# Kernel optimization log

Hardware: AMD Instinct MI355X
Metric: run time of the kernel (lower is better)

Reference implementation:

```python
import jax, jax.numpy as jnp
import numpy as np

N_STATE = 1024
N_HEAD = 16
HEAD_DIM = N_STATE // N_HEAD
SEQLENS = [1024, 896, 768, 640, 512, 384, 896, 1024]  # sum = 6144
TOTAL = sum(SEQLENS)


def setup_inputs() -> dict:
    key = jax.random.key(0)
    ks = jax.random.split(key, 8)
    s = 0.02
    cu = jnp.asarray(np.concatenate([[0], np.cumsum(SEQLENS)]), dtype=jnp.int32)
    return {
        "x": jax.random.normal(ks[0], (TOTAL, N_STATE), jnp.float32),
        "cu_seqlens": cu,
        "Wq": jax.random.normal(ks[1], (N_STATE, N_STATE), jnp.float32) * s,
        "bq": jax.random.normal(ks[2], (N_STATE,), jnp.float32) * s,
        "Wk": jax.random.normal(ks[3], (N_STATE, N_STATE), jnp.float32) * s,
        "Wv": jax.random.normal(ks[4], (N_STATE, N_STATE), jnp.float32) * s,
        "bv": jax.random.normal(ks[5], (N_STATE,), jnp.float32) * s,
        "Wo": jax.random.normal(ks[6], (N_STATE, N_STATE), jnp.float32) * s,
        "bo": jax.random.normal(ks[7], (N_STATE,), jnp.float32) * s,
    }


def reference(x, cu_seqlens, Wq, bq, Wk, Wv, bv, Wo, bo):
    # cu_seqlens is a static (host) quantity in the original (used via .tolist())
    cu = np.asarray(jax.device_get(cu_seqlens))
    seqlens = cu[1:] - cu[:-1]
    B = len(seqlens)
    Lmax = int(seqlens.max())

    q = x @ Wq.T + bq              # [T, n_state]
    k = x @ Wk.T                   # key has no bias
    v = x @ Wv.T + bv

    # static pad/unpad index maps (honoring the ragged structure)
    ar = np.arange(Lmax)
    valid = ar[None, :] < seqlens[:, None]             # [B, Lmax]
    idx = np.where(valid, cu[:-1, None] + ar[None, :], 0)
    unpad_idx = np.nonzero(valid.reshape(-1))[0]       # flat positions of real tokens
    valid_j = jnp.asarray(valid)

    def pad(t):  # [T, n_state] -> [B, Lmax, H, D], zeros in padding
        p = jnp.where(valid_j[:, :, None], t[idx], 0.0)
        return p.reshape(B, Lmax, N_HEAD, HEAD_DIM)

    qp, kp, vp = pad(q), pad(k), pad(v)
    scale = HEAD_DIM ** -0.5
    # torch adds the bool mask (True->1.0) after masked_fill(mask==0, -max):
    # valid keys get +1.0 (softmax-invariant shift), invalid keys get -finfo.max
    big_neg = jnp.finfo(x.dtype).max
    add_mask = jnp.where(valid_j, 1.0, -big_neg)[:, None, None, :]  # [B,1,1,Lmax]

    scores = jnp.einsum("bqhd,bkhd->bhqk", qp, kp) * scale + add_mask
    weights = jax.nn.softmax(scores, axis=-1)
    ctx = jnp.einsum("bhqk,bkhd->bqhd", weights, vp)   # [B, Lmax, H, D]
    ctx_flat = ctx.reshape(B * Lmax, N_STATE)[unpad_idx]  # [T, n_state]
    return ctx_flat @ Wo.T + bo
```

## Files before the change

kernel.cpp:

```cpp
#include <hip/hip_runtime.h>

typedef unsigned short u16;
typedef unsigned int u32;
typedef __attribute__((ext_vector_type(8))) short bf16x8;
typedef __attribute__((ext_vector_type(4))) float f32x4;

#define MFMA_BF16(a, b, c) __builtin_amdgcn_mfma_f32_16x16x32_bf16((a), (b), (c), 0, 0, 0)

#define QSCALE 0.18033688011112042f

__device__ __forceinline__ u16 f2bf(float f) {
    union { float f; unsigned u; } v; v.f = f;
    return (u16)((v.u + 0x7FFFu + ((v.u >> 16) & 1u)) >> 16);
}

__device__ __forceinline__ u32 cvtpk(float a, float b) {
    u32 r;
    asm("v_cvt_pk_bf16_f32 %0, %1, %2" : "=v"(r) : "v"(a), "v"(b));
    return r;
}

__device__ __forceinline__ void async16(const void* g, void* l) {
    __builtin_amdgcn_global_load_lds(
        (const __attribute__((address_space(1))) void*)g,
        (__attribute__((address_space(3))) void*)l, 16, 0, 0);
}

__global__ __launch_bounds__(256) void cvt_all(
    const float* __restrict__ x, const float* __restrict__ Wq, const float* __restrict__ Wk,
    const float* __restrict__ Wv, const float* __restrict__ Wo,
    u16* __restrict__ xb, u16* __restrict__ Wqb, u16* __restrict__ Wkb,
    u16* __restrict__ Wvb, u16* __restrict__ Wob) {
    int b = blockIdx.x;
    const float* src; u16* dst; int base;
    if (b < 6144)      { src = x;  dst = xb;  base = b; }
    else if (b < 7168) { src = Wq; dst = Wqb; base = b - 6144; }
    else if (b < 8192) { src = Wk; dst = Wkb; base = b - 7168; }
    else if (b < 9216) { src = Wv; dst = Wvb; base = b - 8192; }
    else               { src = Wo; dst = Wob; base = b - 9216; }
    int i = base * 256 + threadIdx.x;
    float4 v = ((const float4*)src)[i];
    unsigned long long pk = (unsigned long long)f2bf(v.x)
                          | ((unsigned long long)f2bf(v.y) << 16)
                          | ((unsigned long long)f2bf(v.z) << 32)
                          | ((unsigned long long)f2bf(v.w) << 48);
    *(unsigned long long*)(dst + (size_t)i * 4) = pk;
}

__global__ __launch_bounds__(512) void gemm_qkv(
    const u16* __restrict__ xb,
    const u16* __restrict__ Wqb, const u16* __restrict__ Wkb, const u16* __restrict__ Wvb,
    const float* __restrict__ bq, const float* __restrict__ bv,
    u16* __restrict__ qb, u16* __restrict__ kb, u16* __restrict__ vbT) {
    __shared__ __align__(16) u16 As[2][128 * 64];
    __shared__ __align__(16) u16 Bs[2][128 * 64];
    const int tid = threadIdx.x;

    const int fid = blockIdx.x;
    const int xcd = fid & 7;
    const int slot = fid >> 3;
    const int mloc = slot % 6;
    const int nidx = slot / 6;
    const int m0 = (xcd * 6 + mloc) << 7;
    const int buf = nidx >> 3;
    const int n0 = (nidx & 7) << 7;
    const u16* __restrict__ W = (buf == 0) ? Wqb : (buf == 1) ? Wkb : Wvb;

    const int rr = tid >> 3;
    const int cg = tid & 7;
    const int wv = tid >> 6, lane = tid & 63, g = lane >> 4, c = lane & 15;
    const int wm = (wv & 1) << 6;
    const int wn = (wv >> 1) << 5;

    const int sw = (cg ^ (rr & 7)) << 3;
    const u16* gA[2]; const u16* gB[2];
#pragma unroll
    for (int r = 0; r < 2; ++r) {
        gA[r] = xb + (size_t)(m0 + (r << 6) + rr) * 1024 + sw;
        gB[r] = W + (size_t)(n0 + (r << 6) + rr) * 1024 + sw;
    }

    f32x4 zero = {0.f, 0.f, 0.f, 0.f};
    f32x4 acc[4][2];
#pragma unroll
    for (int i = 0; i < 4; ++i)
#pragma unroll
        for (int j = 0; j < 2; ++j) acc[i][j] = zero;

#pragma unroll
    for (int r = 0; r < 2; ++r) {
        async16(gA[r], &As[0][(r << 12) + tid * 8]);
        async16(gB[r], &Bs[0][(r << 12) + tid * 8]);
    }
#pragma unroll
    for (int r = 0; r < 2; ++r) {
        async16(gA[r] + 64, &As[1][(r << 12) + tid * 8]);
        async16(gB[r] + 64, &Bs[1][(r << 12) + tid * 8]);
    }
    asm volatile("s_waitcnt vmcnt(4)" ::: "memory");
    __builtin_amdgcn_s_barrier();
    __builtin_amdgcn_sched_barrier(0);

    for (int kt = 0; kt < 16; ++kt) {
        const int cur = kt & 1;
#pragma unroll
        for (int ks = 0; ks < 2; ++ks) {
            bf16x8 af[4], bb[2];
#pragma unroll
            for (int i = 0; i < 4; ++i) {
                int ra = wm + (i << 4) + c;
                af[i] = *(const bf16x8*)(&As[cur][ra * 64 + ((((ks << 2) + g) ^ (ra & 7)) << 3)]);
            }
#pragma unroll
            for (int j = 0; j < 2; ++j) {
                int rb = wn + (j << 4) + c;
                bb[j] = *(const bf16x8*)(&Bs[cur][rb * 64 + ((((ks << 2) + g) ^ (rb & 7)) << 3)]);
            }
#pragma unroll
            for (int i = 0; i < 4; ++i)
#pragma unroll
                for (int j = 0; j < 2; ++j) acc[i][j] = MFMA_BF16(af[i], bb[j], acc[i][j]);
        }
        if (kt == 15) break;
        __builtin_amdgcn_sched_barrier(0);
        __builtin_amdgcn_s_barrier();
        if (kt < 14) {
            const int k0 = (kt + 2) << 6;
#pragma unroll
            for (int r = 0; r < 2; ++r) {
                async16(gA[r] + k0, &As[cur][(r << 12) + tid * 8]);
                async16(gB[r] + k0, &Bs[cur][(r << 12) + tid * 8]);
            }
            asm volatile("s_waitcnt vmcnt(4)" ::: "memory");
        } else {
            asm volatile("s_waitcnt vmcnt(0)" ::: "memory");
        }
        __builtin_amdgcn_s_barrier();
        __builtin_amdgcn_sched_barrier(0);
    }

    if (buf == 0) {
#pragma unroll
        for (int j = 0; j < 2; ++j) {
            int col = n0 + wn + (j << 4) + c;
            float bias = bq[col];
#pragma unroll
            for (int i = 0; i < 4; ++i) {
                int rowb = m0 + wm + (i << 4) + (g << 2);
#pragma unroll
                for (int r = 0; r < 4; ++r)
                    qb[(size_t)(rowb + r) * 1024 + col] = f2bf((acc[i][j][r] + bias) * QSCALE);
            }
        }
    } else if (buf == 1) {
#pragma unroll
        for (int j = 0; j < 2; ++j) {
            int col = n0 + wn + (j << 4) + c;
#pragma unroll
            for (int i = 0; i < 4; ++i) {
                int rowb = m0 + wm + (i << 4) + (g << 2);
#pragma unroll
                for (int r = 0; r < 4; ++r)
                    kb[(size_t)(rowb + r) * 1024 + col] = f2bf(acc[i][j][r]);
            }
        }
    } else {
#pragma unroll
        for (int j = 0; j < 2; ++j) {
            int col = n0 + wn + (j << 4) + c;
            float bias = bv[col];
#pragma unroll
            for (int i = 0; i < 4; ++i) {
                int trow = m0 + wm + (i << 4) + (g << 2);
                unsigned long long pk =
                      (unsigned long long)f2bf(acc[i][j][0] + bias)
                    | ((unsigned long long)f2bf(acc[i][j][1] + bias) << 16)
                    | ((unsigned long long)f2bf(acc[i][j][2] + bias) << 32)
                    | ((unsigned long long)f2bf(acc[i][j][3] + bias) << 48);
                *(unsigned long long*)(vbT + (size_t)col * 6144 + trow) = pk;
            }
        }
    }
}

__global__ __launch_bounds__(512) void gemm_out(
    const u16* __restrict__ ctxb, const u16* __restrict__ Wob,
    const float* __restrict__ bo, float* __restrict__ out) {
    __shared__ __align__(16) u16 As[2][128 * 64];
    __shared__ __align__(16) u16 Bs[2][128 * 64];
    const int tid = threadIdx.x;

    const int fid = blockIdx.x;
    const int xcd = fid & 7;
    const int slot = fid >> 3;
    const int mloc = slot % 6;
    const int nidx = slot / 6;
    const int m0 = (xcd * 6 + mloc) << 7;
    const int n0 = nidx << 7;

    const int rr = tid >> 3, cg = tid & 7;
    const int wv = tid >> 6, lane = tid & 63, g = lane >> 4, c = lane & 15;
    const int wm = (wv & 1) << 6;
    const int wn = (wv >> 1) << 5;

    const int sw = (cg ^ (rr & 7)) << 3;
    const u16* gA[2]; const u16* gB[2];
#pragma unroll
    for (int r = 0; r < 2; ++r) {
        gA[r] = ctxb + (size_t)(m0 + (r << 6) + rr) * 1024 + sw;
        gB[r] = Wob + (size_t)(n0 + (r << 6) + rr) * 1024 + sw;
    }

    f32x4 zero = {0.f, 0.f, 0.f, 0.f};
    f32x4 acc[4][2];
#pragma unroll
    for (int i = 0; i < 4; ++i)
#pragma unroll
        for (int j = 0; j < 2; ++j) acc[i][j] = zero;

#pragma unroll
    for (int r = 0; r < 2; ++r) {
        async16(gA[r], &As[0][(r << 12) + tid * 8]);
        async16(gB[r], &Bs[0][(r << 12) + tid * 8]);
    }
#pragma unroll
    for (int r = 0; r < 2; ++r) {
        async16(gA[r] + 64, &As[1][(r << 12) + tid * 8]);
        async16(gB[r] + 64, &Bs[1][(r << 12) + tid * 8]);
    }
    asm volatile("s_waitcnt vmcnt(4)" ::: "memory");
    __builtin_amdgcn_s_barrier();
    __builtin_amdgcn_sched_barrier(0);

    for (int kt = 0; kt < 16; ++kt) {
        const int cur = kt & 1;
#pragma unroll
        for (int ks = 0; ks < 2; ++ks) {
            bf16x8 af[4], bb[2];
#pragma unroll
            for (int i = 0; i < 4; ++i) {
                int ra = wm + (i << 4) + c;
                af[i] = *(const bf16x8*)(&As[cur][ra * 64 + ((((ks << 2) + g) ^ (ra & 7)) << 3)]);
            }
#pragma unroll
            for (int j = 0; j < 2; ++j) {
                int rb = wn + (j << 4) + c;
                bb[j] = *(const bf16x8*)(&Bs[cur][rb * 64 + ((((ks << 2) + g) ^ (rb & 7)) << 3)]);
            }
#pragma unroll
            for (int i = 0; i < 4; ++i)
#pragma unroll
                for (int j = 0; j < 2; ++j) acc[i][j] = MFMA_BF16(af[i], bb[j], acc[i][j]);
        }
        if (kt == 15) break;
        __builtin_amdgcn_sched_barrier(0);
        __builtin_amdgcn_s_barrier();
        if (kt < 14) {
            const int k0 = (kt + 2) << 6;
#pragma unroll
            for (int r = 0; r < 2; ++r) {
                async16(gA[r] + k0, &As[cur][(r << 12) + tid * 8]);
                async16(gB[r] + k0, &Bs[cur][(r << 12) + tid * 8]);
            }
            asm volatile("s_waitcnt vmcnt(4)" ::: "memory");
        } else {
            asm volatile("s_waitcnt vmcnt(0)" ::: "memory");
        }
        __builtin_amdgcn_s_barrier();
        __builtin_amdgcn_sched_barrier(0);
    }

#pragma unroll
    for (int j = 0; j < 2; ++j) {
        int col = n0 + wn + (j << 4) + c;
        float bias = bo[col];
#pragma unroll
        for (int i = 0; i < 4; ++i) {
            int rowb = m0 + wm + (i << 4) + (g << 2);
#pragma unroll
            for (int r = 0; r < 4; ++r)
                out[(size_t)(rowb + r) * 1024 + col] = acc[i][j][r] + bias;
        }
    }
}

__global__ __launch_bounds__(256) void attn_kernel(const u16* __restrict__ qb,
                                                   const u16* __restrict__ kb,
                                                   const u16* __restrict__ vbT,
                                                   u16* __restrict__ ctxb) {
    __shared__ __align__(16) u16 Ks[128 * 64];
    __shared__ __align__(16) u16 Vs[64 * 128];
    __shared__ __align__(16) u16 Ps[4 * 2048];

    const int tid = threadIdx.x;
    const int fid = blockIdx.x;
    const int xcd = fid & 7;
    const int slot = fid >> 3;
    const int h = (xcd << 1) + (slot >= 96 ? 1 : 0);
    const int q0 = (slot % 96) << 6;

    const int cuv[9] = {0, 1024, 1920, 2688, 3328, 3840, 4224, 5120, 6144};
    int s0 = 0, e0 = 6144;
#pragma unroll
    for (int i = 1; i < 8; ++i) {
        if (q0 >= cuv[i]) s0 = cuv[i];
        if (q0 < cuv[i] && cuv[i] < e0) e0 = cuv[i];
    }
    const int ntiles = (e0 - s0) >> 7;

    const int wv = tid >> 6, lane = tid & 63, g = lane >> 4, c = lane & 15;
    const int wrow = wv << 4;

    const u16* qp = qb + (size_t)(q0 + wrow + c) * 1024 + (h << 6) + (g << 3);
    bf16x8 qf0 = *(const bf16x8*)(qp);
    bf16x8 qf1 = *(const bf16x8*)(qp + 32);

    float m_run = -1e30f;
    f32x4 zero = {0.f, 0.f, 0.f, 0.f};
    f32x4 oacc[4];
#pragma unroll
    for (int nt = 0; nt < 4; ++nt) oacc[nt] = zero;
    f32x4 lacc = zero;

    const short one_bf = (short)0x3F80;
    const bf16x8 vones = {one_bf, one_bf, one_bf, one_bf,
                          one_bf, one_bf, one_bf, one_bf};

    const int pbase = (wv << 11) + c * 128;
    const int c7 = c & 7;

    for (int kt = 0; kt < ntiles; ++kt) {
        const int kv0 = s0 + (kt << 7);
        __syncthreads();
        {
            const int rr = tid >> 3, cg = tid & 7;
#pragma unroll
            for (int r = 0; r < 4; ++r) {
                int row = (r << 5) + rr;
                async16(kb + (size_t)(kv0 + row) * 1024 + (h << 6) + ((cg ^ (row & 7)) << 3),
                        Ks + (r << 11) + tid * 8);
            }
            const int rr2 = tid >> 4, cg2 = tid & 15;
#pragma unroll
            for (int r = 0; r < 4; ++r) {
                int row = (r << 4) + rr2;
                async16(vbT + (size_t)((h << 6) + row) * 6144 + kv0 + ((cg2 ^ (row & 15)) << 3),
                        Vs + (r << 11) + tid * 8);
            }
        }
        __syncthreads();

        f32x4 st[8];
#pragma unroll
        for (int mt = 0; mt < 8; ++mt) st[mt] = zero;
        __builtin_amdgcn_s_setprio(1);
#pragma unroll
        for (int mt = 0; mt < 8; ++mt) {
            int row = (mt << 4) + c;
            int sw = row & 7;
            bf16x8 kf0 = *(const bf16x8*)(&Ks[row * 64 + ((g ^ sw) << 3)]);
            bf16x8 kf1 = *(const bf16x8*)(&Ks[row * 64 + (((4 + g) ^ sw) << 3)]);
            st[mt] = MFMA_BF16(kf0, qf0, st[mt]);
            st[mt] = MFMA_BF16(kf1, qf1, st[mt]);
        }
        __builtin_amdgcn_s_setprio(0);

        float mx = fmaxf(fmaxf(st[0][0], st[0][1]), fmaxf(st[0][2], st[0][3]));
#pragma unroll
        for (int mt = 1; mt < 8; ++mt) {
            float a = fmaxf(st[mt][0], fmaxf(st[mt][1], st[mt][2]));
            mx = fmaxf(mx, fmaxf(a, st[mt][3]));
        }
        mx = fmaxf(mx, __shfl_xor(mx, 16, 64));
        mx = fmaxf(mx, __shfl_xor(mx, 32, 64));

        if (!__all(mx - m_run <= 8.f)) {
            float mnew = fmaxf(m_run, mx);
            float alpha = exp2f(m_run - mnew);
            m_run = mnew;
            float al[4];
#pragma unroll
            for (int r = 0; r < 4; ++r) al[r] = __shfl(alpha, (g << 2) + r, 16);
#pragma unroll
            for (int nt = 0; nt < 4; ++nt)
#pragma unroll
                for (int r = 0; r < 4; ++r) oacc[nt][r] *= al[r];
#pragma unroll
            for (int r = 0; r < 4; ++r) lacc[r] *= al[r];
        }

#pragma unroll
        for (int mt = 0; mt < 8; ++mt) {
            float p0 = exp2f(st[mt][0] - m_run);
            float p1 = exp2f(st[mt][1] - m_run);
            float p2 = exp2f(st[mt][2] - m_run);
            float p3 = exp2f(st[mt][3] - m_run);
            int ph = ((mt << 2) + g) ^ (c7 << 1);
            *(uint2*)(Ps + pbase + (ph << 2)) = make_uint2(cvtpk(p0, p1), cvtpk(p2, p3));
        }

        __builtin_amdgcn_s_setprio(1);
#pragma unroll
        for (int ks = 0; ks < 4; ++ks) {
            int pg = ((ks << 2) + g) ^ c7;
            bf16x8 pf = *(const bf16x8*)(Ps + pbase + (pg << 3));
            lacc = MFMA_BF16(pf, vones, lacc);
#pragma unroll
            for (int nt = 0; nt < 4; ++nt) {
                int vrow = (nt << 4) + c;
                bf16x8 vf = *(const bf16x8*)(&Vs[vrow * 128 + ((((ks << 2) + g) ^ (vrow & 15)) << 3)]);
                oacc[nt] = MFMA_BF16(pf, vf, oacc[nt]);
            }
        }
        __builtin_amdgcn_s_setprio(0);
    }

    float invr[4];
#pragma unroll
    for (int r = 0; r < 4; ++r) invr[r] = 1.0f / lacc[r];
#pragma unroll
    for (int r = 0; r < 4; ++r) {
        size_t rowoff = (size_t)(q0 + wrow + (g << 2) + r) * 1024 + (h << 6);
#pragma unroll
        for (int nt = 0; nt < 4; ++nt)
            ctxb[rowoff + (nt << 4) + c] = f2bf(oacc[nt][r] * invr[r]);
    }
}

extern "C" void kernel_launch(void* const* d_in, const int* in_sizes, int n_in,
                              void* d_out, int out_size, void* d_ws, size_t ws_size,
                              hipStream_t stream) {
    const float* x  = (const float*)d_in[0];
    const float* Wq = (const float*)d_in[2];
    const float* bq = (const float*)d_in[3];
    const float* Wk = (const float*)d_in[4];
    const float* Wv = (const float*)d_in[5];
    const float* bv = (const float*)d_in[6];
    const float* Wo = (const float*)d_in[7];
    const float* bo = (const float*)d_in[8];
    float* out = (float*)d_out;

    u16* ws = (u16*)d_ws;
    u16* xb   = ws;
    u16* Wqb  = xb + 6291456;
    u16* Wkb  = Wqb + 1048576;
    u16* Wvb  = Wkb + 1048576;
    u16* Wob  = Wvb + 1048576;
    u16* qb   = Wob + 1048576;
    u16* kb   = qb + 6291456;
    u16* vbT  = kb + 6291456;
    u16* ctxb = xb;

    cvt_all<<<10240, 256, 0, stream>>>(x, Wq, Wk, Wv, Wo, xb, Wqb, Wkb, Wvb, Wob);
    gemm_qkv<<<1152, 512, 0, stream>>>(xb, Wqb, Wkb, Wvb, bq, bv, qb, kb, vbT);
    attn_kernel<<<1536, 256, 0, stream>>>(qb, kb, vbT, ctxb);
    gemm_out<<<384, 512, 0, stream>>>(ctxb, Wob, bo, out);
}
```

Measured before the change: 213.3 us.

## Process two 64-row query tiles per attention block to reuse K/V loads

Each attention workgroup now handles 128 query rows, as two 64-row halves that share every K/V tile staged in LDS, and the grid is halved to 768 blocks. The aim is to halve the global-to-LDS K/V traffic and the barrier count per query row. In exchange each wave holds twice the accumulator registers, which may reduce occupancy, and there are fewer blocks to spread across CUs. All sequence boundaries are multiples of 128, so the segment lookup stays valid.

Result: slower. 225.0 us (+5.5%).

```diff
diff --git a/kernel.cpp b/kernel.cpp
--- a/kernel.cpp
+++ b/kernel.cpp
@@ -296,8 +296,8 @@
     const int fid = blockIdx.x;
     const int xcd = fid & 7;
     const int slot = fid >> 3;
-    const int h = (xcd << 1) + (slot >= 96 ? 1 : 0);
-    const int q0 = (slot % 96) << 6;
+    const int h = (xcd << 1) + (slot >= 48 ? 1 : 0);
+    const int q0 = (slot % 48) << 7;
 
     const int cuv[9] = {0, 1024, 1920, 2688, 3328, 3840, 4224, 5120, 6144};
     int s0 = 0, e0 = 6144;
@@ -311,16 +311,19 @@
     const int wv = tid >> 6, lane = tid & 63, g = lane >> 4, c = lane & 15;
     const int wrow = wv << 4;
 
-    const u16* qp = qb + (size_t)(q0 + wrow + c) * 1024 + (h << 6) + (g << 3);
-    bf16x8 qf0 = *(const bf16x8*)(qp);
-    bf16x8 qf1 = *(const bf16x8*)(qp + 32);
-
-    float m_run = -1e30f;
+    const u16* qpA = qb + (size_t)(q0 + wrow + c) * 1024 + (h << 6) + (g << 3);
+    const u16* qpB = qpA + (size_t)64 * 1024;
+    bf16x8 qA0 = *(const bf16x8*)(qpA);
+    bf16x8 qA1 = *(const bf16x8*)(qpA + 32);
+    bf16x8 qB0 = *(const bf16x8*)(qpB);
+    bf16x8 qB1 = *(const bf16x8*)(qpB + 32);
+
     f32x4 zero = {0.f, 0.f, 0.f, 0.f};
-    f32x4 oacc[4];
-#pragma unroll
-    for (int nt = 0; nt < 4; ++nt) oacc[nt] = zero;
-    f32x4 lacc = zero;
+    float mA = -1e30f, mB = -1e30f;
+    f32x4 oA[4], oB[4];
+#pragma unroll
+    for (int nt = 0; nt < 4; ++nt) { oA[nt] = zero; oB[nt] = zero; }
+    f32x4 lA = zero, lB = zero;
 
     const short one_bf = (short)0x3F80;
     const bf16x8 vones = {one_bf, one_bf, one_bf, one_bf,
@@ -329,27 +332,8 @@
     const int pbase = (wv << 11) + c * 128;
     const int c7 = c & 7;
 
-    for (int kt = 0; kt < ntiles; ++kt) {
-        const int kv0 = s0 + (kt << 7);
-        __syncthreads();
-        {
-            const int rr = tid >> 3, cg = tid & 7;
-#pragma unroll
-            for (int r = 0; r < 4; ++r) {
-                int row = (r << 5) + rr;
-                async16(kb + (size_t)(kv0 + row) * 1024 + (h << 6) + ((cg ^ (row & 7)) << 3),
-                        Ks + (r << 11) + tid * 8);
-            }
-            const int rr2 = tid >> 4, cg2 = tid & 15;
-#pragma unroll
-            for (int r = 0; r < 4; ++r) {
-                int row = (r << 4) + rr2;
-                async16(vbT + (size_t)((h << 6) + row) * 6144 + kv0 + ((cg2 ^ (row & 15)) << 3),
-                        Vs + (r << 11) + tid * 8);
-            }
-        }
-        __syncthreads();
-
+    auto half = [&](const bf16x8& qf0, const bf16x8& qf1,
+                    float& m_run, f32x4& lacc, f32x4* oacc) {
         f32x4 st[8];
 #pragma unroll
         for (int mt = 0; mt < 8; ++mt) st[mt] = zero;
@@ -413,17 +397,45 @@
             }
         }
         __builtin_amdgcn_s_setprio(0);
-    }
-
-    float invr[4];
-#pragma unroll
-    for (int r = 0; r < 4; ++r) invr[r] = 1.0f / lacc[r];
+    };
+
+    for (int kt = 0; kt < ntiles; ++kt) {
+        const int kv0 = s0 + (kt << 7);
+        __syncthreads();
+        {
+            const int rr = tid >> 3, cg = tid & 7;
+#pragma unroll
+            for (int r = 0; r < 4; ++r) {
+                int row = (r << 5) + rr;
+                async16(kb + (size_t)(kv0 + row) * 1024 + (h << 6) + ((cg ^ (row & 7)) << 3),
+                        Ks + (r << 11) + tid * 8);
+            }
+            const int rr2 = tid >> 4, cg2 = tid & 15;
+#pragma unroll
+            for (int r = 0; r < 4; ++r) {
+                int row = (r << 4) + rr2;
+                async16(vbT + (size_t)((h << 6) + row) * 6144 + kv0 + ((cg2 ^ (row & 15)) << 3),
+                        Vs + (r << 11) + tid * 8);
+            }
+        }
+        __syncthreads();
+
+        half(qA0, qA1, mA, lA, oA);
+        half(qB0, qB1, mB, lB, oB);
+    }
+
+    float invA[4], invB[4];
+#pragma unroll
+    for (int r = 0; r < 4; ++r) { invA[r] = 1.0f / lA[r]; invB[r] = 1.0f / lB[r]; }
 #pragma unroll
     for (int r = 0; r < 4; ++r) {
-        size_t rowoff = (size_t)(q0 + wrow + (g << 2) + r) * 1024 + (h << 6);
-#pragma unroll
-        for (int nt = 0; nt < 4; ++nt)
-            ctxb[rowoff + (nt << 4) + c] = f2bf(oacc[nt][r] * invr[r]);
+        size_t rowA = (size_t)(q0 + wrow + (g << 2) + r) * 1024 + (h << 6);
+        size_t rowB = rowA + (size_t)64 * 1024;
+#pragma unroll
+        for (int nt = 0; nt < 4; ++nt) {
+            ctxb[rowA + (nt << 4) + c] = f2bf(oA[nt][r] * invA[r]);
+            ctxb[rowB + (nt << 4) + c] = f2bf(oB[nt][r] * invB[r]);
+        }
     }
 }
 
@@ -453,6 +465,6 @@
 
     cvt_all<<<10240, 256, 0, stream>>>(x, Wq, Wk, Wv, Wo, xb, Wqb, Wkb, Wvb, Wob);
     gemm_qkv<<<1152, 512, 0, stream>>>(xb, Wqb, Wkb, Wvb, bq, bv, qb, kb, vbT);
-    attn_kernel<<<1536, 256, 0, stream>>>(qb, kb, vbT, ctxb);
+    attn_kernel<<<768, 256, 0, stream>>>(qb, kb, vbT, ctxb);
     gemm_out<<<384, 512, 0, stream>>>(ctxb, Wob, bo, out);
 }
```
